# Kernel optimization log

Measured on AMD Instinct MI355X. Metric: run time of the kernel, lower is better.

The kernel has to match this reference:

```python
import jax, jax.numpy as jnp
import numpy as np

N_NODES = 100000
N_EDGES = 1600000
D_IN = 16
D_HID = 32   # 2 * out_channels
D_OUT = 16


def gcn_conv(h, src, dst, W, b, num_nodes):
    """PyG-style GCNConv: x' = D^{-1/2} (A+I) D^{-1/2} (x W) + b.
    src/dst already include self-loops."""
    h = h @ W                                   # [N, F_out] linear transform first
    deg = jnp.zeros((num_nodes,), h.dtype).at[dst].add(1.0)
    dinv = jax.lax.rsqrt(jnp.maximum(deg, 1.0))  # deg >= 1 due to self-loops
    norm = dinv[src] * dinv[dst]                # [E+N]
    msg = h[src] * norm[:, None]                # edge gather (memory-bound)
    out = jax.ops.segment_sum(msg, dst, num_segments=num_nodes)
    return out + b


def setup_inputs() -> dict:
    key = jax.random.key(0)
    k1, k2, k3, k4 = jax.random.split(key, 4)
    x = jnp.arange(N_NODES, dtype=jnp.int32)
    edge_index = jax.random.randint(k1, (2, N_EDGES), 0, N_NODES, dtype=jnp.int32)
    emb = jax.random.normal(k2, (N_NODES, D_IN), dtype=jnp.float32)
    W1 = jax.random.normal(k3, (D_IN, D_HID), dtype=jnp.float32) * (1.0 / np.sqrt(D_IN))
    b1 = jnp.zeros((D_HID,), jnp.float32)
    W2 = jax.random.normal(k4, (D_HID, D_OUT), dtype=jnp.float32) * (1.0 / np.sqrt(D_HID))
    b2 = jnp.zeros((D_OUT,), jnp.float32)
    return {"x": x, "edge_index": edge_index, "emb": emb,
            "W1": W1, "b1": b1, "W2": W2, "b2": b2}


def reference(x, edge_index, emb, W1, b1, W2, b2):
    num_nodes = emb.shape[0]
    # add self-loops once; reused by both conv layers
    loops = jnp.arange(num_nodes, dtype=edge_index.dtype)
    src = jnp.concatenate([edge_index[0], loops])
    dst = jnp.concatenate([edge_index[1], loops])

    h = emb[x]                                  # embedding lookup
    h = jax.nn.relu(gcn_conv(h, src, dst, W1, b1, num_nodes))
    # dropout is identity in eval mode (reference baseline)
    out = gcn_conv(h, src, dst, W2, b2, num_nodes)
    return out
```

## Files before the change

kernel.cpp:

```cpp
#include <hip/hip_runtime.h>


#define BS   256
#define NBLK 256
#define BINSHIFT 8
#define BIN  256
#define MAXBINS 512
#define BINCAP 4608

union H2 { int i; _Float16 h[2]; };

__global__ void k_hist(const int* __restrict__ dst, int E, int NBINS,
                       int* __restrict__ histG) {
    __shared__ int h[MAXBINS];
    int t = threadIdx.x;
    for (int i = t; i < NBINS; i += BS) h[i] = 0;
    __syncthreads();
    int E4 = E >> 2;
    const int4* d4 = (const int4*)dst;
    for (int i = blockIdx.x * BS + t; i < E4; i += NBLK * BS) {
        int4 d = d4[i];
        atomicAdd(&h[d.x >> BINSHIFT], 1);
        atomicAdd(&h[d.y >> BINSHIFT], 1);
        atomicAdd(&h[d.z >> BINSHIFT], 1);
        atomicAdd(&h[d.w >> BINSHIFT], 1);
    }
    if (blockIdx.x == 0 && t < (E & 3))
        atomicAdd(&h[dst[(E4 << 2) + t] >> BINSHIFT], 1);
    __syncthreads();
    for (int i = t; i < NBINS; i += BS) histG[i * NBLK + blockIdx.x] = h[i];
}

__global__ void k_scanA(const int* __restrict__ in, int L,
                        int* __restrict__ partial, int* __restrict__ bsum) {
    __shared__ int s[BS];
    int t = threadIdx.x;
    int i = blockIdx.x * BS + t;
    int v = (i < L) ? in[i] : 0;
    s[t] = v;
    __syncthreads();
    for (int off = 1; off < BS; off <<= 1) {
        int add = (t >= off) ? s[t - off] : 0;
        __syncthreads();
        s[t] += add;
        __syncthreads();
    }
    if (i < L) partial[i] = s[t] - v;
    if (t == BS - 1) bsum[blockIdx.x] = s[BS - 1];
}

__global__ void k_scanB(const int* __restrict__ bsum, int nB, int* __restrict__ boff) {
    __shared__ int s[BS];
    int t = threadIdx.x;
    int PER = (nB + BS - 1) / BS;
    int loc[8];
    int base = t * PER;
    int sum = 0;
    for (int j = 0; j < PER && j < 8; j++) {
        int idx = base + j;
        int v = (idx < nB) ? bsum[idx] : 0;
        loc[j] = sum;
        sum += v;
    }
    s[t] = sum;
    __syncthreads();
    for (int off = 1; off < BS; off <<= 1) {
        int add = (t >= off) ? s[t - off] : 0;
        __syncthreads();
        s[t] += add;
        __syncthreads();
    }
    int ex = s[t] - sum;
    for (int j = 0; j < PER && j < 8; j++) {
        int idx = base + j;
        if (idx < nB) boff[idx] = ex + loc[j];
    }
}

__global__ void k_binscatter(const int* __restrict__ src, const int* __restrict__ dst,
                             int E, int NBINS, const int* __restrict__ partial,
                             const int* __restrict__ boff, int* __restrict__ packed) {
    __shared__ int cur[MAXBINS];
    int t = threadIdx.x;
    for (int i = t; i < NBINS; i += BS)
        cur[i] = partial[i * NBLK + blockIdx.x] + boff[i];
    __syncthreads();
    int E4 = E >> 2;
    const int4* s4 = (const int4*)src;
    const int4* d4 = (const int4*)dst;
    for (int i = blockIdx.x * BS + t; i < E4; i += NBLK * BS) {
        int4 s = s4[i];
        int4 d = d4[i];
        int p0 = atomicAdd(&cur[d.x >> BINSHIFT], 1);
        packed[p0] = s.x | ((d.x & (BIN - 1)) << 18);
        int p1 = atomicAdd(&cur[d.y >> BINSHIFT], 1);
        packed[p1] = s.y | ((d.y & (BIN - 1)) << 18);
        int p2 = atomicAdd(&cur[d.z >> BINSHIFT], 1);
        packed[p2] = s.z | ((d.z & (BIN - 1)) << 18);
        int p3 = atomicAdd(&cur[d.w >> BINSHIFT], 1);
        packed[p3] = s.w | ((d.w & (BIN - 1)) << 18);
    }
    if (blockIdx.x == 0 && t < (E & 3)) {
        int e = (E4 << 2) + t;
        int d = dst[e];
        int p = atomicAdd(&cur[d >> BINSHIFT], 1);
        packed[p] = src[e] | ((d & (BIN - 1)) << 18);
    }
}

__global__ void k_binsort(const int* __restrict__ packed,
                          const int* __restrict__ partial, const int* __restrict__ boff,
                          int NBINS, int N, int E,
                          const int* __restrict__ x, const float* __restrict__ emb,
                          const float* __restrict__ W1,
                          int* __restrict__ row_start, float* __restrict__ dinv,
                          int* __restrict__ col, _Float16* __restrict__ sig1) {
    __shared__ int buf[BINCAP];
    __shared__ int ldeg[BIN];
    __shared__ int lrs[BIN];
    __shared__ int cur[BIN];
    __shared__ float sW[512];
    int b = blockIdx.x;
    int t = threadIdx.x;
    int node0 = b << BINSHIFT;
    int e0 = partial[b * NBLK] + boff[b];
    int e1 = (b + 1 < NBINS) ? (partial[(b + 1) * NBLK] + boff[b + 1]) : E;
    int cnt = e1 - e0;
    bool fits = (cnt <= BINCAP);
    if (b == 0 && t == 0) row_start[N] = E;
    sW[t] = W1[t];
    sW[t + 256] = W1[t + 256];
    ldeg[t] = 0;
    if (fits)
        for (int i = t; i < cnt; i += BS) buf[i] = packed[e0 + i];
    __syncthreads();
    for (int i = t; i < cnt; i += BS) {
        int v = fits ? buf[i] : packed[e0 + i];
        atomicAdd(&ldeg[((unsigned)v >> 18) & (BIN - 1)], 1);
    }
    __syncthreads();
    lrs[t] = ldeg[t];
    __syncthreads();
    for (int off = 1; off < BIN; off <<= 1) {
        int add = (t >= off) ? lrs[t - off] : 0;
        __syncthreads();
        lrs[t] += add;
        __syncthreads();
    }
    int myDeg = ldeg[t];
    int ex = lrs[t] - myDeg;
    cur[t] = ex;
    int n = node0 + t;
    float di = rsqrtf((float)(myDeg + 1));
    if (n < N) {
        row_start[n] = e0 + ex;
        dinv[n] = di;
    }
    __syncthreads();
    for (int i = t; i < cnt; i += BS) {
        int v = fits ? buf[i] : packed[e0 + i];
        int pos = atomicAdd(&cur[((unsigned)v >> 18) & (BIN - 1)], 1);
        col[e0 + pos] = v & 0x3FFFF;
    }
    if (n < N) {
        const float4* er = (const float4*)(emb + (size_t)x[n] * 16);
        float4 ra = er[0], rb = er[1], rc = er[2], rd = er[3];
        float ev[16] = {ra.x, ra.y, ra.z, ra.w, rb.x, rb.y, rb.z, rb.w,
                        rc.x, rc.y, rc.z, rc.w, rd.x, rd.y, rd.z, rd.w};
        int4* s1o = (int4*)sig1;
        #pragma unroll
        for (int cq = 0; cq < 4; cq++) {
            H2 pk[4];
            #pragma unroll
            for (int dw = 0; dw < 4; dw++) {
                int c = cq * 8 + dw * 2;
                float acc0 = 0.f, acc1 = 0.f;
                #pragma unroll
                for (int k = 0; k < 16; k++) {
                    acc0 += ev[k] * sW[k * 32 + c];
                    acc1 += ev[k] * sW[k * 32 + c + 1];
                }
                pk[dw].h[0] = (_Float16)(acc0 * di);
                pk[dw].h[1] = (_Float16)(acc1 * di);
            }
            int4 pv;
            pv.x = pk[0].i; pv.y = pk[1].i; pv.z = pk[2].i; pv.w = pk[3].i;
            s1o[(size_t)n * 4 + cq] = pv;
        }
    }
}

__global__ __launch_bounds__(BS) void k_agg1mm2(
    const _Float16* __restrict__ sig1, const int* __restrict__ row_start,
    const float* __restrict__ dinv, const int* __restrict__ col,
    const float* __restrict__ b1, const float* __restrict__ W2,
    int N, _Float16* __restrict__ sig2) {
    __shared__ float sW[32][17];
    int t = threadIdx.x;
    sW[t >> 4][t & 15] = W2[t];
    sW[(t >> 4) + 16][t & 15] = W2[t + 256];
    __syncthreads();
    int lane = t & 63;
    int n = blockIdx.x * (BS / 64) + (t >> 6);
    if (n >= N) return;
    int g  = lane >> 4;
    int cd = lane & 15;
    const int* s1i = (const int*)sig1;
    int rs = __builtin_amdgcn_readfirstlane(row_start[n]);
    int re = __builtin_amdgcn_readfirstlane(row_start[n + 1]);
    int dn = re - rs;
    float a0 = 0.f, a1 = 0.f;
    int iters = (dn + 15) >> 4;
    int colv = 0;
    if (iters > 0) {
        int idx = cd; if (idx > dn - 1) idx = dn - 1;
        colv = col[rs + idx];
    }
    for (int it = 0; it < iters; it++) {
        int e = it << 4;
        int coln = 0;
        if (it + 1 < iters) {
            int idx = e + 16 + cd; if (idx > dn - 1) idx = dn - 1;
            coln = col[rs + idx];
        }
        int s0 = __shfl(colv, g);
        int s1 = __shfl(colv, 4 + g);
        int s2 = __shfl(colv, 8 + g);
        int s3 = __shfl(colv, 12 + g);
        H2 u0, u1, u2, u3;
        u0.i = s1i[s0 * 16 + cd];
        u1.i = s1i[s1 * 16 + cd];
        u2.i = s1i[s2 * 16 + cd];
        u3.i = s1i[s3 * 16 + cd];
        float m0 = (e + g      < dn) ? 1.f : 0.f;
        float m1 = (e + 4 + g  < dn) ? 1.f : 0.f;
        float m2 = (e + 8 + g  < dn) ? 1.f : 0.f;
        float m3 = (e + 12 + g < dn) ? 1.f : 0.f;
        a0 += (m0 * (float)u0.h[0] + m1 * (float)u1.h[0])
            + (m2 * (float)u2.h[0] + m3 * (float)u3.h[0]);
        a1 += (m0 * (float)u0.h[1] + m1 * (float)u1.h[1])
            + (m2 * (float)u2.h[1] + m3 * (float)u3.h[1]);
        colv = coln;
    }
    a0 += __shfl_xor(a0, 16); a0 += __shfl_xor(a0, 32);
    a1 += __shfl_xor(a1, 16); a1 += __shfl_xor(a1, 32);
    H2 us; us.i = s1i[n * 16 + cd];
    a0 += (float)us.h[0];
    a1 += (float)us.h[1];
    float di = dinv[n];
    float2 b = ((const float2*)b1)[cd];
    float h0 = fmaxf(a0 * di + b.x, 0.f);
    float h1 = fmaxf(a1 * di + b.y, 0.f);
    float a = 0.f;
    #pragma unroll
    for (int j = 0; j < 4; j++) {
        int cdk = 4 * g + j;
        float hk0 = __shfl(h0, cdk);
        float hk1 = __shfl(h1, cdk);
        a += hk0 * sW[2 * cdk][cd] + hk1 * sW[2 * cdk + 1][cd];
    }
    a += __shfl_xor(a, 16);
    a += __shfl_xor(a, 32);
    if (lane < 16) sig2[n * 16 + cd] = (_Float16)(a * di);
}

__global__ __launch_bounds__(BS) void k_agg2(
    const _Float16* __restrict__ sig2, const int* __restrict__ row_start,
    const float* __restrict__ dinv, const int* __restrict__ col,
    const float* __restrict__ b2, int N, float* __restrict__ out) {
    int t = threadIdx.x;
    int lane = t & 63;
    int n = blockIdx.x * (BS / 64) + (t >> 6);
    if (n >= N) return;
    int g  = lane >> 3;
    int cd = lane & 7;
    const int* s2i = (const int*)sig2;
    int rs = __builtin_amdgcn_readfirstlane(row_start[n]);
    int re = __builtin_amdgcn_readfirstlane(row_start[n + 1]);
    int dn = re - rs;
    float a0 = 0.f, a1 = 0.f;
    int iters = (dn + 31) >> 5;
    int l32 = lane & 31;
    int colv = 0;
    if (iters > 0) {
        int idx = l32; if (idx > dn - 1) idx = dn - 1;
        colv = col[rs + idx];
    }
    for (int it = 0; it < iters; it++) {
        int e = it << 5;
        int coln = 0;
        if (it + 1 < iters) {
            int idx = e + 32 + l32; if (idx > dn - 1) idx = dn - 1;
            coln = col[rs + idx];
        }
        int s0 = __shfl(colv, g);
        int s1 = __shfl(colv, 8 + g);
        int s2 = __shfl(colv, 16 + g);
        int s3 = __shfl(colv, 24 + g);
        H2 u0, u1, u2, u3;
        u0.i = s2i[s0 * 8 + cd];
        u1.i = s2i[s1 * 8 + cd];
        u2.i = s2i[s2 * 8 + cd];
        u3.i = s2i[s3 * 8 + cd];
        float m0 = (e + g      < dn) ? 1.f : 0.f;
        float m1 = (e + 8 + g  < dn) ? 1.f : 0.f;
        float m2 = (e + 16 + g < dn) ? 1.f : 0.f;
        float m3 = (e + 24 + g < dn) ? 1.f : 0.f;
        a0 += (m0 * (float)u0.h[0] + m1 * (float)u1.h[0])
            + (m2 * (float)u2.h[0] + m3 * (float)u3.h[0]);
        a1 += (m0 * (float)u0.h[1] + m1 * (float)u1.h[1])
            + (m2 * (float)u2.h[1] + m3 * (float)u3.h[1]);
        colv = coln;
    }
    a0 += __shfl_xor(a0, 8); a0 += __shfl_xor(a0, 16); a0 += __shfl_xor(a0, 32);
    a1 += __shfl_xor(a1, 8); a1 += __shfl_xor(a1, 16); a1 += __shfl_xor(a1, 32);
    H2 us; us.i = s2i[n * 8 + cd];
    a0 += (float)us.h[0];
    a1 += (float)us.h[1];
    if (lane < 8) {
        float di = dinv[n];
        float2 b = ((const float2*)b2)[cd];
        float2 o;
        o.x = a0 * di + b.x;
        o.y = a1 * di + b.y;
        ((float2*)out)[n * 8 + cd] = o;
    }
}

extern "C" void kernel_launch(void* const* d_in, const int* in_sizes, int n_in,
                              void* d_out, int out_size, void* d_ws, size_t ws_size,
                              hipStream_t stream) {
    const int*   x   = (const int*)d_in[0];
    const int*   ei  = (const int*)d_in[1];
    const float* emb = (const float*)d_in[2];
    const float* W1  = (const float*)d_in[3];
    const float* b1  = (const float*)d_in[4];
    const float* W2  = (const float*)d_in[5];
    const float* b2  = (const float*)d_in[6];
    float* out = (float*)d_out;

    const int N = in_sizes[0];
    const int E = in_sizes[1] / 2;
    const int* srcp = ei;
    const int* dstp = ei + E;
    const int NBINS = (N + BIN - 1) >> BINSHIFT;
    const int L = NBINS * NBLK;
    const int nB2 = (L + BS - 1) / BS;

    auto al = [](size_t b) { return (b + 255) & ~size_t(255); };
    char* w = (char*)d_ws;
    auto carve = [&](size_t bytes) {
        void* p = (void*)w;
        w += al(bytes);
        return p;
    };
    int*   row_start = (int*)carve((size_t)(N + 1) * 4);
    float* dinv      = (float*)carve((size_t)N * 4);
    int*   col       = (int*)carve((size_t)E * 4);
    int*   histG     = (int*)carve((size_t)L * 4);
    int*   partial   = (int*)carve((size_t)L * 4);
    int*   bsum      = (int*)carve((size_t)nB2 * 4);
    int*   boff      = (int*)carve((size_t)nB2 * 4);
    int*   packed    = (int*)carve((size_t)E * 4);
    _Float16* sig1   = (_Float16*)carve((size_t)N * 32 * 2);
    _Float16* sig2   = (_Float16*)carve((size_t)N * 16 * 2);
    (void)ws_size; (void)n_in; (void)out_size;

    int gL = (L + BS - 1) / BS;
    k_hist<<<NBLK, BS, 0, stream>>>(dstp, E, NBINS, histG);
    k_scanA<<<gL, BS, 0, stream>>>(histG, L, partial, bsum);
    k_scanB<<<1, BS, 0, stream>>>(bsum, nB2, boff);
    k_binscatter<<<NBLK, BS, 0, stream>>>(srcp, dstp, E, NBINS, partial, boff, packed);
    k_binsort<<<NBINS, BS, 0, stream>>>(packed, partial, boff, NBINS, N, E,
                                        x, emb, W1, row_start, dinv, col, sig1);

    int gW = (N + 3) / 4;
    k_agg1mm2<<<gW, BS, 0, stream>>>(sig1, row_start, dinv, col, b1, W2, N, sig2);
    k_agg2<<<gW, BS, 0, stream>>>(sig2, row_start, dinv, col, b2, N, out);
}
```

Measured before the change: 180.8 us.

## Map four nodes per wavefront in aggregation kernels and keep W2 in registers

Both aggregation kernels now give each wavefront four destination nodes instead of one, with 16 lanes per node, so low-degree rows (about 17 edges on average) waste fewer lanes and need fewer cross-lane reductions. Each 16-lane group walks its own row in steps of four edges (eight for layer 2), and the loop count is the maximum degree across the wave. The layer-2 matmul now holds W2 columns in registers and reads the hidden vector through a small shared buffer, replacing shuffles. The column prefetch is dropped and lanes idle when degrees differ within a wave; the extra register use may lower occupancy.

```diff
diff --git a/kernel.cpp b/kernel.cpp
--- a/kernel.cpp
+++ b/kernel.cpp
@@ -195,73 +195,71 @@
     const float* __restrict__ dinv, const int* __restrict__ col,
     const float* __restrict__ b1, const float* __restrict__ W2,
     int N, _Float16* __restrict__ sig2) {
-    __shared__ float sW[32][17];
-    int t = threadIdx.x;
-    sW[t >> 4][t & 15] = W2[t];
-    sW[(t >> 4) + 16][t & 15] = W2[t + 256];
-    __syncthreads();
+    __shared__ float hbuf[4][4][36];
+    int t = threadIdx.x;
     int lane = t & 63;
-    int n = blockIdx.x * (BS / 64) + (t >> 6);
-    if (n >= N) return;
+    int wid = t >> 6;
     int g  = lane >> 4;
     int cd = lane & 15;
+    int n = blockIdx.x * 16 + wid * 4 + g;
+    int nld = (n < N) ? n : N - 1;
+    int rs = row_start[nld];
+    int re = row_start[nld + 1];
+    int dn = (n < N) ? (re - rs) : 0;
+    int dnm1 = (dn > 0) ? dn - 1 : 0;
+    int dm = dn;
+    dm = max(dm, __shfl_xor(dm, 16));
+    dm = max(dm, __shfl_xor(dm, 32));
+    float w2c[32];
+    #pragma unroll
+    for (int k = 0; k < 32; k++) w2c[k] = W2[k * 16 + cd];
     const int* s1i = (const int*)sig1;
-    int rs = __builtin_amdgcn_readfirstlane(row_start[n]);
-    int re = __builtin_amdgcn_readfirstlane(row_start[n + 1]);
-    int dn = re - rs;
     float a0 = 0.f, a1 = 0.f;
-    int iters = (dn + 15) >> 4;
-    int colv = 0;
-    if (iters > 0) {
-        int idx = cd; if (idx > dn - 1) idx = dn - 1;
-        colv = col[rs + idx];
-    }
+    int iters = (dm + 3) >> 2;
+    int slot = cd & 3;
+    int bidx = lane & 48;
     for (int it = 0; it < iters; it++) {
-        int e = it << 4;
-        int coln = 0;
-        if (it + 1 < iters) {
-            int idx = e + 16 + cd; if (idx > dn - 1) idx = dn - 1;
-            coln = col[rs + idx];
-        }
-        int s0 = __shfl(colv, g);
-        int s1 = __shfl(colv, 4 + g);
-        int s2 = __shfl(colv, 8 + g);
-        int s3 = __shfl(colv, 12 + g);
-        H2 u0, u1, u2, u3;
-        u0.i = s1i[s0 * 16 + cd];
-        u1.i = s1i[s1 * 16 + cd];
-        u2.i = s1i[s2 * 16 + cd];
-        u3.i = s1i[s3 * 16 + cd];
-        float m0 = (e + g      < dn) ? 1.f : 0.f;
-        float m1 = (e + 4 + g  < dn) ? 1.f : 0.f;
-        float m2 = (e + 8 + g  < dn) ? 1.f : 0.f;
-        float m3 = (e + 12 + g < dn) ? 1.f : 0.f;
-        a0 += (m0 * (float)u0.h[0] + m1 * (float)u1.h[0])
-            + (m2 * (float)u2.h[0] + m3 * (float)u3.h[0]);
-        a1 += (m0 * (float)u0.h[1] + m1 * (float)u1.h[1])
-            + (m2 * (float)u2.h[1] + m3 * (float)u3.h[1]);
-        colv = coln;
-    }
-    a0 += __shfl_xor(a0, 16); a0 += __shfl_xor(a0, 32);
-    a1 += __shfl_xor(a1, 16); a1 += __shfl_xor(a1, 32);
-    H2 us; us.i = s1i[n * 16 + cd];
-    a0 += (float)us.h[0];
-    a1 += (float)us.h[1];
-    float di = dinv[n];
+        int e = it << 2;
+        int idx = e + slot; if (idx > dnm1) idx = dnm1;
+        int colv = col[rs + idx];
+        int s0 = __shfl(colv, bidx + 0);
+        int s1 = __shfl(colv, bidx + 1);
+        int s2 = __shfl(colv, bidx + 2);
+        int s3 = __shfl(colv, bidx + 3);
+        int u0 = s1i[s0 * 16 + cd];
+        int u1 = s1i[s1 * 16 + cd];
+        int u2 = s1i[s2 * 16 + cd];
+        int u3 = s1i[s3 * 16 + cd];
+        u0 = (e + 0 < dn) ? u0 : 0;
+        u1 = (e + 1 < dn) ? u1 : 0;
+        u2 = (e + 2 < dn) ? u2 : 0;
+        u3 = (e + 3 < dn) ? u3 : 0;
+        H2 p0, p1, p2, p3;
+        p0.i = u0; p1.i = u1; p2.i = u2; p3.i = u3;
+        a0 += ((float)p0.h[0] + (float)p1.h[0]) + ((float)p2.h[0] + (float)p3.h[0]);
+        a1 += ((float)p0.h[1] + (float)p1.h[1]) + ((float)p2.h[1] + (float)p3.h[1]);
+    }
+    {
+        H2 p; p.i = s1i[nld * 16 + cd];
+        a0 += (float)p.h[0];
+        a1 += (float)p.h[1];
+    }
+    float di = dinv[nld];
     float2 b = ((const float2*)b1)[cd];
     float h0 = fmaxf(a0 * di + b.x, 0.f);
     float h1 = fmaxf(a1 * di + b.y, 0.f);
+    float* hb = hbuf[wid][g];
+    *(float2*)&hb[2 * cd] = make_float2(h0, h1);
     float a = 0.f;
     #pragma unroll
-    for (int j = 0; j < 4; j++) {
-        int cdk = 4 * g + j;
-        float hk0 = __shfl(h0, cdk);
-        float hk1 = __shfl(h1, cdk);
-        a += hk0 * sW[2 * cdk][cd] + hk1 * sW[2 * cdk + 1][cd];
-    }
-    a += __shfl_xor(a, 16);
-    a += __shfl_xor(a, 32);
-    if (lane < 16) sig2[n * 16 + cd] = (_Float16)(a * di);
+    for (int k = 0; k < 32; k += 4) {
+        float4 hv = *(const float4*)&hb[k];
+        a = fmaf(hv.x, w2c[k],     a);
+        a = fmaf(hv.y, w2c[k + 1], a);
+        a = fmaf(hv.z, w2c[k + 2], a);
+        a = fmaf(hv.w, w2c[k + 3], a);
+    }
+    if (n < N) sig2[(size_t)n * 16 + cd] = (_Float16)(a * di);
 }
 
 __global__ __launch_bounds__(BS) void k_agg2(
@@ -270,60 +268,52 @@
     const float* __restrict__ b2, int N, float* __restrict__ out) {
     int t = threadIdx.x;
     int lane = t & 63;
-    int n = blockIdx.x * (BS / 64) + (t >> 6);
-    if (n >= N) return;
-    int g  = lane >> 3;
+    int g  = lane >> 4;
+    int e2 = (lane >> 3) & 1;
     int cd = lane & 7;
+    int n = blockIdx.x * 16 + (t >> 6) * 4 + g;
+    int nld = (n < N) ? n : N - 1;
+    int rs = row_start[nld];
+    int re = row_start[nld + 1];
+    int dn = (n < N) ? (re - rs) : 0;
+    int dnm1 = (dn > 0) ? dn - 1 : 0;
+    int dm = dn;
+    dm = max(dm, __shfl_xor(dm, 16));
+    dm = max(dm, __shfl_xor(dm, 32));
     const int* s2i = (const int*)sig2;
-    int rs = __builtin_amdgcn_readfirstlane(row_start[n]);
-    int re = __builtin_amdgcn_readfirstlane(row_start[n + 1]);
-    int dn = re - rs;
     float a0 = 0.f, a1 = 0.f;
-    int iters = (dn + 31) >> 5;
-    int l32 = lane & 31;
-    int colv = 0;
-    if (iters > 0) {
-        int idx = l32; if (idx > dn - 1) idx = dn - 1;
-        colv = col[rs + idx];
-    }
+    int iters = (dm + 7) >> 3;
+    int slot = lane & 7;
+    int bidx = lane & 48;
     for (int it = 0; it < iters; it++) {
-        int e = it << 5;
-        int coln = 0;
-        if (it + 1 < iters) {
-            int idx = e + 32 + l32; if (idx > dn - 1) idx = dn - 1;
-            coln = col[rs + idx];
+        int e = it << 3;
+        int idx = e + slot; if (idx > dnm1) idx = dnm1;
+        int colv = col[rs + idx];
+        #pragma unroll
+        for (int j = 0; j < 4; j++) {
+            int sl = 2 * j + e2;
+            int sv = __shfl(colv, bidx + sl);
+            int u = s2i[sv * 8 + cd];
+            u = (e + sl < dn) ? u : 0;
+            H2 p; p.i = u;
+            a0 += (float)p.h[0];
+            a1 += (float)p.h[1];
         }
-        int s0 = __shfl(colv, g);
-        int s1 = __shfl(colv, 8 + g);
-        int s2 = __shfl(colv, 16 + g);
-        int s3 = __shfl(colv, 24 + g);
-        H2 u0, u1, u2, u3;
-        u0.i = s2i[s0 * 8 + cd];
-        u1.i = s2i[s1 * 8 + cd];
-        u2.i = s2i[s2 * 8 + cd];
-        u3.i = s2i[s3 * 8 + cd];
-        float m0 = (e + g      < dn) ? 1.f : 0.f;
-        float m1 = (e + 8 + g  < dn) ? 1.f : 0.f;
-        float m2 = (e + 16 + g < dn) ? 1.f : 0.f;
-        float m3 = (e + 24 + g < dn) ? 1.f : 0.f;
-        a0 += (m0 * (float)u0.h[0] + m1 * (float)u1.h[0])
-            + (m2 * (float)u2.h[0] + m3 * (float)u3.h[0]);
-        a1 += (m0 * (float)u0.h[1] + m1 * (float)u1.h[1])
-            + (m2 * (float)u2.h[1] + m3 * (float)u3.h[1]);
-        colv = coln;
-    }
-    a0 += __shfl_xor(a0, 8); a0 += __shfl_xor(a0, 16); a0 += __shfl_xor(a0, 32);
-    a1 += __shfl_xor(a1, 8); a1 += __shfl_xor(a1, 16); a1 += __shfl_xor(a1, 32);
-    H2 us; us.i = s2i[n * 8 + cd];
-    a0 += (float)us.h[0];
-    a1 += (float)us.h[1];
-    if (lane < 8) {
-        float di = dinv[n];
+    }
+    a0 += __shfl_xor(a0, 8);
+    a1 += __shfl_xor(a1, 8);
+    {
+        H2 p; p.i = s2i[nld * 8 + cd];
+        a0 += (float)p.h[0];
+        a1 += (float)p.h[1];
+    }
+    if (n < N && e2 == 0) {
+        float di = dinv[nld];
         float2 b = ((const float2*)b2)[cd];
         float2 o;
         o.x = a0 * di + b.x;
         o.y = a1 * di + b.y;
-        ((float2*)out)[n * 8 + cd] = o;
+        ((float2*)out)[(size_t)n * 8 + cd] = o;
     }
 }
 
@@ -356,7 +346,7 @@
     };
     int*   row_start = (int*)carve((size_t)(N + 1) * 4);
     float* dinv      = (float*)carve((size_t)N * 4);
-    int*   col       = (int*)carve((size_t)E * 4);
+    int*   col       = (int*)carve((size_t)(E + 256) * 4);
     int*   histG     = (int*)carve((size_t)L * 4);
     int*   partial   = (int*)carve((size_t)L * 4);
     int*   bsum      = (int*)carve((size_t)nB2 * 4);
@@ -374,7 +364,7 @@
     k_binsort<<<NBINS, BS, 0, stream>>>(packed, partial, boff, NBINS, N, E,
                                         x, emb, W1, row_start, dinv, col, sig1);
 
-    int gW = (N + 3) / 4;
-    k_agg1mm2<<<gW, BS, 0, stream>>>(sig1, row_start, dinv, col, b1, W2, N, sig2);
-    k_agg2<<<gW, BS, 0, stream>>>(sig2, row_start, dinv, col, b2, N, out);
-}
+    int gA = (N + 15) / 16;
+    k_agg1mm2<<<gA, BS, 0, stream>>>(sig1, row_start, dinv, col, b1, W2, N, sig2);
+    k_agg2<<<gA, BS, 0, stream>>>(sig2, row_start, dinv, col, b2, N, out);
+}
```

After: 159.4 us. 11.9% less time.
